# Optimization experiments

Measured on AMD Instinct MI355X. Metric: run time of the kernel, lower is better.

Reference implementation:

```python
import jax, jax.numpy as jnp
import numpy as np


def setup_inputs() -> dict:
    key = jax.random.key(0)
    ks = jax.random.split(key, 7)
    B = 65536
    x = jax.random.normal(ks[0], (B, 1, 28, 28), dtype=jnp.float32)
    conv_w = jax.random.normal(ks[1], (4, 1, 7, 7), dtype=jnp.float32) * 0.1
    conv_b = jax.random.normal(ks[2], (4,), dtype=jnp.float32) * 0.1
    fc1_w = jax.random.normal(ks[3], (64, 256), dtype=jnp.float32) * 0.05
    fc1_b = jax.random.normal(ks[4], (64,), dtype=jnp.float32) * 0.05
    fc2_w = jax.random.normal(ks[5], (10, 64), dtype=jnp.float32) * 0.1
    fc2_b = jax.random.normal(ks[6], (10,), dtype=jnp.float32) * 0.1
    return {"x": x, "conv_w": conv_w, "conv_b": conv_b,
            "fc1_w": fc1_w, "fc1_b": fc1_b, "fc2_w": fc2_w, "fc2_b": fc2_b}


def reference(x, conv_w, conv_b, fc1_w, fc1_b, fc2_w, fc2_b):
    # conv1: 1->4 channels, 7x7 kernel, stride 3, no padding -> [B,4,8,8]
    h = jax.lax.conv_general_dilated(
        x, conv_w, window_strides=(3, 3), padding="VALID",
        dimension_numbers=("NCHW", "OIHW", "NCHW"))
    h = h + conv_b[None, :, None, None]
    h = h * h  # SquareFunction (CKKS polynomial activation)
    h = h.reshape(h.shape[0], -1)  # [B, 256]
    h = jnp.einsum("bi,oi->bo", h, fc1_w) + fc1_b
    h = h * h  # SquareFunction
    out = jnp.einsum("bi,oi->bo", h, fc2_w) + fc2_b  # [B, 10]
    return out
```

## Files before the change

kernel.cpp:

```cpp
#include <hip/hip_runtime.h>


#define BLK_IMGS    64
#define CHUNK_IMGS  8
#define NCHUNK      8
#define XCH_FLOATS  (CHUNK_IMGS * 784)

#define LDS_XBUF    0
#define LDS_H       12544
#define LDS_H2      28928
#define LDS_W2      33024
#define LDS_OUT     34048
#define LDS_TOTAL_F 34688

__global__ __launch_bounds__(512, 2)
void encconv_fused2(const float* __restrict__ x,
                    const float* __restrict__ conv_w,
                    const float* __restrict__ conv_b,
                    const float* __restrict__ fc1_w,
                    const float* __restrict__ fc1_b,
                    const float* __restrict__ fc2_w,
                    const float* __restrict__ fc2_b,
                    float* __restrict__ out)
{
    extern __shared__ float lds[];
    float*  xbuf = lds + LDS_XBUF;
    float4* hb   = (float4*)(lds + LDS_H);
    float4* h2b  = (float4*)(lds + LDS_H2);
    float4* w2b  = (float4*)(lds + LDS_W2);
    float*  ob   = lds + LDS_OUT;

    const int tid = threadIdx.x;
    const int blk = blockIdx.x;
    const long base_img = (long)blk * BLK_IMGS;

    const int g  = tid >> 6;
    const int y  = (tid >> 3) & 7;
    const int c  = (tid >> 1) & 3;
    const int xh = tid & 1;

    float wv[49];
    #pragma unroll
    for (int i = 0; i < 49; ++i) wv[i] = conv_w[c * 49 + i];
    const float cb = conv_b[c];

    if (tid < 160) {
        float4 v = *(const float4*)(fc2_w + tid * 4);
        int e  = tid * 4;
        int j  = e >> 6;
        int kk = (e & 63) >> 2;
        w2b[kk * 16 + j] = v;
    }

    const float* xblk = x + base_img * 784;

    float4 pf0, pf1, pf2, pf3;
    {
        const float* src = xblk;
        pf0 = *(const float4*)(src + 4 * tid);
        pf1 = *(const float4*)(src + 4 * (tid + 512));
        pf2 = *(const float4*)(src + 4 * (tid + 1024));
        if (tid < 32) pf3 = *(const float4*)(src + 4 * (tid + 1536));
    }

    for (int ch = 0; ch < NCHUNK; ++ch) {
        float* xb = xbuf + (ch & 1) * XCH_FLOATS;

        *(float4*)(xb + 4 * tid)          = pf0;
        *(float4*)(xb + 4 * (tid + 512))  = pf1;
        *(float4*)(xb + 4 * (tid + 1024)) = pf2;
        if (tid < 32) *(float4*)(xb + 4 * (tid + 1536)) = pf3;
        __syncthreads();

        if (ch + 1 < NCHUNK) {
            const float* src = xblk + (ch + 1) * XCH_FLOATS;
            pf0 = *(const float4*)(src + 4 * tid);
            pf1 = *(const float4*)(src + 4 * (tid + 512));
            pf2 = *(const float4*)(src + 4 * (tid + 1024));
            if (tid < 32) pf3 = *(const float4*)(src + 4 * (tid + 1536));
        }

        float acc0 = 0.f, acc1 = 0.f, acc2 = 0.f, acc3 = 0.f;
        const float* xi = xb + g * 784;
        #pragma unroll
        for (int rr = 0; rr < 7; ++rr) {
            const float* rp = xi + (3 * y + rr) * 28 + 12 * xh;
            float4 r0 = *(const float4*)(rp + 0);
            float4 r1 = *(const float4*)(rp + 4);
            float4 r2 = *(const float4*)(rp + 8);
            float4 r3 = *(const float4*)(rp + 12);
            float r[16] = { r0.x, r0.y, r0.z, r0.w,
                            r1.x, r1.y, r1.z, r1.w,
                            r2.x, r2.y, r2.z, r2.w,
                            r3.x, r3.y, r3.z, r3.w };
            #pragma unroll
            for (int kx = 0; kx < 7; ++kx) {
                const float w = wv[rr * 7 + kx];
                acc0 = fmaf(r[0 + kx], w, acc0);
                acc1 = fmaf(r[3 + kx], w, acc1);
                acc2 = fmaf(r[6 + kx], w, acc2);
                acc3 = fmaf(r[9 + kx], w, acc3);
            }
        }

        float4 hv;
        hv.x = acc0 + cb; hv.x *= hv.x;
        hv.y = acc1 + cb; hv.y *= hv.y;
        hv.z = acc2 + cb; hv.z *= hv.z;
        hv.w = acc3 + cb; hv.w *= hv.w;
        hb[(c * 16 + y * 2 + xh) * 64 + (ch * CHUNK_IMGS + g)] = hv;
    }
    __syncthreads();

    {
        const int img = tid & 63;
        const int w8  = __builtin_amdgcn_readfirstlane(tid >> 6);
        const float* wbase = fc1_w + (w8 * 8) * 256;

        float a0=0.f,a1=0.f,a2=0.f,a3=0.f,a4=0.f,a5=0.f,a6=0.f,a7=0.f;

        #pragma unroll 2
        for (int k4 = 0; k4 < 64; ++k4) {
            float4 h4 = hb[k4 * 64 + img];
            const float* wp = wbase + k4 * 4;
            float4 w0 = *(const float4*)(wp + 0 * 256);
            float4 w1 = *(const float4*)(wp + 1 * 256);
            float4 w2 = *(const float4*)(wp + 2 * 256);
            float4 w3 = *(const float4*)(wp + 3 * 256);
            float4 w4 = *(const float4*)(wp + 4 * 256);
            float4 w5 = *(const float4*)(wp + 5 * 256);
            float4 w6 = *(const float4*)(wp + 6 * 256);
            float4 w7 = *(const float4*)(wp + 7 * 256);
            a0 = fmaf(h4.x,w0.x,a0); a0 = fmaf(h4.y,w0.y,a0); a0 = fmaf(h4.z,w0.z,a0); a0 = fmaf(h4.w,w0.w,a0);
            a1 = fmaf(h4.x,w1.x,a1); a1 = fmaf(h4.y,w1.y,a1); a1 = fmaf(h4.z,w1.z,a1); a1 = fmaf(h4.w,w1.w,a1);
            a2 = fmaf(h4.x,w2.x,a2); a2 = fmaf(h4.y,w2.y,a2); a2 = fmaf(h4.z,w2.z,a2); a2 = fmaf(h4.w,w2.w,a2);
            a3 = fmaf(h4.x,w3.x,a3); a3 = fmaf(h4.y,w3.y,a3); a3 = fmaf(h4.z,w3.z,a3); a3 = fmaf(h4.w,w3.w,a3);
            a4 = fmaf(h4.x,w4.x,a4); a4 = fmaf(h4.y,w4.y,a4); a4 = fmaf(h4.z,w4.z,a4); a4 = fmaf(h4.w,w4.w,a4);
            a5 = fmaf(h4.x,w5.x,a5); a5 = fmaf(h4.y,w5.y,a5); a5 = fmaf(h4.z,w5.z,a5); a5 = fmaf(h4.w,w5.w,a5);
            a6 = fmaf(h4.x,w6.x,a6); a6 = fmaf(h4.y,w6.y,a6); a6 = fmaf(h4.z,w6.z,a6); a6 = fmaf(h4.w,w6.w,a6);
            a7 = fmaf(h4.x,w7.x,a7); a7 = fmaf(h4.y,w7.y,a7); a7 = fmaf(h4.z,w7.z,a7); a7 = fmaf(h4.w,w7.w,a7);
        }

        const float* bp = fc1_b + w8 * 8;
        float4 p0, p1;
        p0.x = a0 + bp[0]; p0.x *= p0.x;
        p0.y = a1 + bp[1]; p0.y *= p0.y;
        p0.z = a2 + bp[2]; p0.z *= p0.z;
        p0.w = a3 + bp[3]; p0.w *= p0.w;
        p1.x = a4 + bp[4]; p1.x *= p1.x;
        p1.y = a5 + bp[5]; p1.y *= p1.y;
        p1.z = a6 + bp[6]; p1.z *= p1.z;
        p1.w = a7 + bp[7]; p1.w *= p1.w;
        h2b[(w8 * 2 + 0) * 64 + img] = p0;
        h2b[(w8 * 2 + 1) * 64 + img] = p1;
    }
    __syncthreads();

    {
        const int im3 = tid >> 3;
        const int q   = tid & 7;

        float s1 = 0.f;
        #pragma unroll
        for (int k4 = 0; k4 < 16; ++k4) {
            float4 hh = h2b[k4 * 64 + im3];
            float4 wA = w2b[k4 * 16 + q];
            s1 = fmaf(hh.x, wA.x, s1); s1 = fmaf(hh.y, wA.y, s1);
            s1 = fmaf(hh.z, wA.z, s1); s1 = fmaf(hh.w, wA.w, s1);
        }
        ob[im3 * 10 + q] = s1 + fc2_b[q];

        if (q < 2) {
            float s2 = 0.f;
            #pragma unroll
            for (int k4 = 0; k4 < 16; ++k4) {
                float4 hh = h2b[k4 * 64 + im3];
                float4 wB = w2b[k4 * 16 + 8 + q];
                s2 = fmaf(hh.x, wB.x, s2); s2 = fmaf(hh.y, wB.y, s2);
                s2 = fmaf(hh.z, wB.z, s2); s2 = fmaf(hh.w, wB.w, s2);
            }
            ob[im3 * 10 + 8 + q] = s2 + fc2_b[8 + q];
        }
    }
    __syncthreads();

    if (tid < 160) {
        float4 v = *(const float4*)(ob + tid * 4);
        *(float4*)(out + (long)blk * 640 + tid * 4) = v;
    }
}

extern "C" void kernel_launch(void* const* d_in, const int* in_sizes, int n_in,
                              void* d_out, int out_size, void* d_ws, size_t ws_size,
                              hipStream_t stream) {
    const float* x      = (const float*)d_in[0];
    const float* conv_w = (const float*)d_in[1];
    const float* conv_b = (const float*)d_in[2];
    const float* fc1_w  = (const float*)d_in[3];
    const float* fc1_b  = (const float*)d_in[4];
    const float* fc2_w  = (const float*)d_in[5];
    const float* fc2_b  = (const float*)d_in[6];
    float* out = (float*)d_out;

    const int B = in_sizes[0] / 784;
    const int blocks = (B + BLK_IMGS - 1) / BLK_IMGS;
    const size_t lds_bytes = LDS_TOTAL_F * sizeof(float);

    static bool attr_set = false;
    if (!attr_set) {
        (void)hipFuncSetAttribute((const void*)encconv_fused2,
                                  hipFuncAttributeMaxDynamicSharedMemorySize,
                                  (int)lds_bytes);
        attr_set = true;
    }

    encconv_fused2<<<blocks, 512, lds_bytes, stream>>>(
        x, conv_w, conv_b, fc1_w, fc1_b, fc2_w, fc2_b, out);
}
```

Measured before the change: 358.4 us.

## Shrink LDS footprint with fp16 conv activations and buffer aliasing for occupancy

Conv outputs are stored in LDS as packed fp16 instead of fp32, and rows are XOR-swizzled to avoid bank conflicts. The input staging buffer goes from double to single buffering, and the fc1 and fc2 scratch regions are aliased onto it, with extra barriers added to keep them safe. Together this cuts LDS per block from about 139KB to about 62KB, and launch bounds are raised to 4 blocks per CU to increase occupancy. The cost is more barriers per chunk, fp16 rounding error in the fc1 input, and register pressure from the 49-weight array under the tighter launch bound.

```diff
diff --git a/kernel.cpp b/kernel.cpp
--- a/kernel.cpp
+++ b/kernel.cpp
@@ -1,4 +1,5 @@
 #include <hip/hip_runtime.h>
+#include <hip/hip_fp16.h>
 
 
 #define BLK_IMGS    64
@@ -7,14 +8,14 @@
 #define XCH_FLOATS  (CHUNK_IMGS * 784)
 
 #define LDS_XBUF    0
-#define LDS_H       12544
-#define LDS_H2      28928
-#define LDS_W2      33024
-#define LDS_OUT     34048
-#define LDS_TOTAL_F 34688
-
-__global__ __launch_bounds__(512, 2)
-void encconv_fused2(const float* __restrict__ x,
+#define LDS_H_F     6272
+#define LDS_W2_F    (6272 + 8192)
+#define LDS_TOTAL_F (6272 + 8192 + 1024)
+
+union h2cvt { __half2 h; unsigned int u; };
+
+__global__ __launch_bounds__(512, 4)
+void encconv_fused3(const float* __restrict__ x,
                     const float* __restrict__ conv_w,
                     const float* __restrict__ conv_b,
                     const float* __restrict__ fc1_w,
@@ -25,10 +26,10 @@
 {
     extern __shared__ float lds[];
     float*  xbuf = lds + LDS_XBUF;
-    float4* hb   = (float4*)(lds + LDS_H);
-    float4* h2b  = (float4*)(lds + LDS_H2);
-    float4* w2b  = (float4*)(lds + LDS_W2);
-    float*  ob   = lds + LDS_OUT;
+    uint2*  hbuf = (uint2*)(lds + LDS_H_F);
+    float4* w2b  = (float4*)(lds + LDS_W2_F);
+    float4* h2b  = (float4*)(lds + LDS_XBUF);
+    float*  ob   = lds + 4096;
 
     const int tid = threadIdx.x;
     const int blk = blockIdx.x;
@@ -38,6 +39,8 @@
     const int y  = (tid >> 3) & 7;
     const int c  = (tid >> 1) & 3;
     const int xh = tid & 1;
+    const int k4 = c * 16 + y * 2 + xh;
+    const int sw = (y * 2 + xh) & 15;
 
     float wv[49];
     #pragma unroll
@@ -64,12 +67,11 @@
     }
 
     for (int ch = 0; ch < NCHUNK; ++ch) {
-        float* xb = xbuf + (ch & 1) * XCH_FLOATS;
-
-        *(float4*)(xb + 4 * tid)          = pf0;
-        *(float4*)(xb + 4 * (tid + 512))  = pf1;
-        *(float4*)(xb + 4 * (tid + 1024)) = pf2;
-        if (tid < 32) *(float4*)(xb + 4 * (tid + 1536)) = pf3;
+        if (ch > 0) __syncthreads();
+        *(float4*)(xbuf + 4 * tid)          = pf0;
+        *(float4*)(xbuf + 4 * (tid + 512))  = pf1;
+        *(float4*)(xbuf + 4 * (tid + 1024)) = pf2;
+        if (tid < 32) *(float4*)(xbuf + 4 * (tid + 1536)) = pf3;
         __syncthreads();
 
         if (ch + 1 < NCHUNK) {
@@ -81,7 +83,7 @@
         }
 
         float acc0 = 0.f, acc1 = 0.f, acc2 = 0.f, acc3 = 0.f;
-        const float* xi = xb + g * 784;
+        const float* xi = xbuf + g * 784;
         #pragma unroll
         for (int rr = 0; rr < 7; ++rr) {
             const float* rp = xi + (3 * y + rr) * 28 + 12 * xh;
@@ -103,12 +105,15 @@
             }
         }
 
-        float4 hv;
-        hv.x = acc0 + cb; hv.x *= hv.x;
-        hv.y = acc1 + cb; hv.y *= hv.y;
-        hv.z = acc2 + cb; hv.z *= hv.z;
-        hv.w = acc3 + cb; hv.w *= hv.w;
-        hb[(c * 16 + y * 2 + xh) * 64 + (ch * CHUNK_IMGS + g)] = hv;
+        float h0 = acc0 + cb; h0 *= h0;
+        float h1 = acc1 + cb; h1 *= h1;
+        float h2v_ = acc2 + cb; h2v_ *= h2v_;
+        float h3 = acc3 + cb; h3 *= h3;
+        h2cvt lo, hi;
+        lo.h = __floats2half2_rn(h0, h1);
+        hi.h = __floats2half2_rn(h2v_, h3);
+        const int img = ch * CHUNK_IMGS + g;
+        hbuf[(k4 << 6) + (img ^ sw)] = make_uint2(lo.u, hi.u);
     }
     __syncthreads();
 
@@ -120,9 +125,12 @@
         float a0=0.f,a1=0.f,a2=0.f,a3=0.f,a4=0.f,a5=0.f,a6=0.f,a7=0.f;
 
         #pragma unroll 2
-        for (int k4 = 0; k4 < 64; ++k4) {
-            float4 h4 = hb[k4 * 64 + img];
-            const float* wp = wbase + k4 * 4;
+        for (int kk = 0; kk < 64; ++kk) {
+            uint2 hu = hbuf[(kk << 6) + (img ^ (kk & 15))];
+            h2cvt ua, ub; ua.u = hu.x; ub.u = hu.y;
+            float2 f01 = __half22float2(ua.h);
+            float2 f23 = __half22float2(ub.h);
+            const float* wp = wbase + kk * 4;
             float4 w0 = *(const float4*)(wp + 0 * 256);
             float4 w1 = *(const float4*)(wp + 1 * 256);
             float4 w2 = *(const float4*)(wp + 2 * 256);
@@ -131,15 +139,17 @@
             float4 w5 = *(const float4*)(wp + 5 * 256);
             float4 w6 = *(const float4*)(wp + 6 * 256);
             float4 w7 = *(const float4*)(wp + 7 * 256);
-            a0 = fmaf(h4.x,w0.x,a0); a0 = fmaf(h4.y,w0.y,a0); a0 = fmaf(h4.z,w0.z,a0); a0 = fmaf(h4.w,w0.w,a0);
-            a1 = fmaf(h4.x,w1.x,a1); a1 = fmaf(h4.y,w1.y,a1); a1 = fmaf(h4.z,w1.z,a1); a1 = fmaf(h4.w,w1.w,a1);
-            a2 = fmaf(h4.x,w2.x,a2); a2 = fmaf(h4.y,w2.y,a2); a2 = fmaf(h4.z,w2.z,a2); a2 = fmaf(h4.w,w2.w,a2);
-            a3 = fmaf(h4.x,w3.x,a3); a3 = fmaf(h4.y,w3.y,a3); a3 = fmaf(h4.z,w3.z,a3); a3 = fmaf(h4.w,w3.w,a3);
-            a4 = fmaf(h4.x,w4.x,a4); a4 = fmaf(h4.y,w4.y,a4); a4 = fmaf(h4.z,w4.z,a4); a4 = fmaf(h4.w,w4.w,a4);
-            a5 = fmaf(h4.x,w5.x,a5); a5 = fmaf(h4.y,w5.y,a5); a5 = fmaf(h4.z,w5.z,a5); a5 = fmaf(h4.w,w5.w,a5);
-            a6 = fmaf(h4.x,w6.x,a6); a6 = fmaf(h4.y,w6.y,a6); a6 = fmaf(h4.z,w6.z,a6); a6 = fmaf(h4.w,w6.w,a6);
-            a7 = fmaf(h4.x,w7.x,a7); a7 = fmaf(h4.y,w7.y,a7); a7 = fmaf(h4.z,w7.z,a7); a7 = fmaf(h4.w,w7.w,a7);
-        }
+            a0 = fmaf(f01.x,w0.x,a0); a0 = fmaf(f01.y,w0.y,a0); a0 = fmaf(f23.x,w0.z,a0); a0 = fmaf(f23.y,w0.w,a0);
+            a1 = fmaf(f01.x,w1.x,a1); a1 = fmaf(f01.y,w1.y,a1); a1 = fmaf(f23.x,w1.z,a1); a1 = fmaf(f23.y,w1.w,a1);
+            a2 = fmaf(f01.x,w2.x,a2); a2 = fmaf(f01.y,w2.y,a2); a2 = fmaf(f23.x,w2.z,a2); a2 = fmaf(f23.y,w2.w,a2);
+            a3 = fmaf(f01.x,w3.x,a3); a3 = fmaf(f01.y,w3.y,a3); a3 = fmaf(f23.x,w3.z,a3); a3 = fmaf(f23.y,w3.w,a3);
+            a4 = fmaf(f01.x,w4.x,a4); a4 = fmaf(f01.y,w4.y,a4); a4 = fmaf(f23.x,w4.z,a4); a4 = fmaf(f23.y,w4.w,a4);
+            a5 = fmaf(f01.x,w5.x,a5); a5 = fmaf(f01.y,w5.y,a5); a5 = fmaf(f23.x,w5.z,a5); a5 = fmaf(f23.y,w5.w,a5);
+            a6 = fmaf(f01.x,w6.x,a6); a6 = fmaf(f01.y,w6.y,a6); a6 = fmaf(f23.x,w6.z,a6); a6 = fmaf(f23.y,w6.w,a6);
+            a7 = fmaf(f01.x,w7.x,a7); a7 = fmaf(f01.y,w7.y,a7); a7 = fmaf(f23.x,w7.z,a7); a7 = fmaf(f23.y,w7.w,a7);
+        }
+
+        __syncthreads();
 
         const float* bp = fc1_b + w8 * 8;
         float4 p0, p1;
@@ -162,25 +172,29 @@
 
         float s1 = 0.f;
         #pragma unroll
-        for (int k4 = 0; k4 < 16; ++k4) {
-            float4 hh = h2b[k4 * 64 + im3];
-            float4 wA = w2b[k4 * 16 + q];
+        for (int kk = 0; kk < 16; ++kk) {
+            float4 hh = h2b[kk * 64 + im3];
+            float4 wA = w2b[kk * 16 + q];
             s1 = fmaf(hh.x, wA.x, s1); s1 = fmaf(hh.y, wA.y, s1);
             s1 = fmaf(hh.z, wA.z, s1); s1 = fmaf(hh.w, wA.w, s1);
         }
-        ob[im3 * 10 + q] = s1 + fc2_b[q];
-
+        float r1 = s1 + fc2_b[q];
+
+        float r2 = 0.f;
         if (q < 2) {
             float s2 = 0.f;
             #pragma unroll
-            for (int k4 = 0; k4 < 16; ++k4) {
-                float4 hh = h2b[k4 * 64 + im3];
-                float4 wB = w2b[k4 * 16 + 8 + q];
+            for (int kk = 0; kk < 16; ++kk) {
+                float4 hh = h2b[kk * 64 + im3];
+                float4 wB = w2b[kk * 16 + 8 + q];
                 s2 = fmaf(hh.x, wB.x, s2); s2 = fmaf(hh.y, wB.y, s2);
                 s2 = fmaf(hh.z, wB.z, s2); s2 = fmaf(hh.w, wB.w, s2);
             }
-            ob[im3 * 10 + 8 + q] = s2 + fc2_b[8 + q];
-        }
+            r2 = s2 + fc2_b[8 + q];
+        }
+        __syncthreads();
+        ob[im3 * 10 + q] = r1;
+        if (q < 2) ob[im3 * 10 + 8 + q] = r2;
     }
     __syncthreads();
 
@@ -208,12 +222,12 @@
 
     static bool attr_set = false;
     if (!attr_set) {
-        (void)hipFuncSetAttribute((const void*)encconv_fused2,
+        (void)hipFuncSetAttribute((const void*)encconv_fused3,
                                   hipFuncAttributeMaxDynamicSharedMemorySize,
                                   (int)lds_bytes);
         attr_set = true;
     }
 
-    encconv_fused2<<<blocks, 512, lds_bytes, stream>>>(
+    encconv_fused3<<<blocks, 512, lds_bytes, stream>>>(
         x, conv_w, conv_b, fc1_w, fc1_b, fc2_w, fc2_b, out);
 }
```

Result: slower. 488.9 us (+36.4%).
